# Kernel tuning notes

Measured on AMD Instinct MI355X. Metric: run time of the kernel, lower is better.

## Reference

```python
import jax, jax.numpy as jnp
import numpy as np

B, T, H = 8, 2048, 2048


def _wkv(key, value, time_decay, time_first):
    # key, value: [B, T, H]; time_decay/time_first: [H]
    u = time_first
    w = -jnp.exp(time_decay)  # negative decay per channel

    a0 = jnp.zeros(key.shape[::2], key.dtype)            # [B, H]
    b0 = jnp.zeros_like(a0)
    e0 = jnp.full_like(a0, -jnp.inf)

    def step(carry, kv):
        a, b, exponent = carry
        kt, vt = kv                                       # [B, H] each
        # output for this timestep (numerically stabilized)
        max_exp = jnp.maximum(exponent, u + kt)
        wt = jnp.exp(u + kt - max_exp)
        scale = jnp.exp(exponent - max_exp)
        wkv = (a * scale + wt * vt) / (b * scale + wt)
        # state update with decay w
        max_exp2 = jnp.maximum(exponent + w, kt)
        s1 = jnp.exp(exponent + w - max_exp2)
        s2 = jnp.exp(kt - max_exp2)
        a = s1 * a + s2 * vt
        b = s1 * b + s2
        return (a, b, max_exp2), wkv

    kT = jnp.swapaxes(key, 0, 1)    # [T, B, H] for scan over time
    vT = jnp.swapaxes(value, 0, 1)
    _, out = jax.lax.scan(step, (a0, b0, e0), (kT, vT))
    return jnp.swapaxes(out, 0, 1)  # [B, T, H]


def setup_inputs() -> dict:
    key = jax.random.key(0)
    k1, k2, k3, k4 = jax.random.split(key, 4)
    return {
        "key": jax.random.normal(k1, (B, T, H), jnp.float32),
        "value": jax.random.normal(k2, (B, T, H), jnp.float32),
        "time_decay": jax.random.normal(k3, (H,), jnp.float32) * 0.5,
        "time_first": jax.random.normal(k4, (H,), jnp.float32) * 0.5,
    }


def reference(key, value, time_decay, time_first):
    return _wkv(key, value, time_decay, time_first)
```

## Files before the change

kernel.cpp:

```cpp
#include <hip/hip_runtime.h>
#include <math.h>


#define WKV_B 8
#define WKV_T 2048
#define WKV_H 2048
#define WKV_BH (WKV_B * WKV_H)
#define WKV_U 8

__device__ __forceinline__ void wkv_update(float& a, float& bs, float& e,
                                           float w, float kt, float vt) {
    float ew = e + w;
    float m2 = fmaxf(ew, kt);
    float s1 = __expf(ew - m2);
    float s2 = __expf(kt - m2);
    a  = fmaf(s1, a, s2 * vt);
    bs = fmaf(s1, bs, s2);
    e  = m2;
}

__global__ __launch_bounds__(256)
void wkv_pass1(const float* __restrict__ k_, const float* __restrict__ v_,
               const float* __restrict__ td,
               float* __restrict__ pa, float* __restrict__ pb,
               float* __restrict__ pe, int L)
{
    const int ch = blockIdx.x * 256 + threadIdx.x;
    const int c  = blockIdx.y;
    const int h  = ch & (WKV_H - 1);
    const int b  = ch >> 11;
    const float w = -__expf(td[h]);

    const size_t base = (size_t)b * WKV_T * WKV_H + h + (size_t)c * L * WKV_H;
    const float* kp = k_ + base;
    const float* vp = v_ + base;

    float a = 0.0f, bs = 0.0f, e = -INFINITY;

    float kA[WKV_U], vA[WKV_U], kB[WKV_U], vB[WKV_U];
    #pragma unroll
    for (int i = 0; i < WKV_U; ++i) {
        kA[i] = kp[(size_t)i * WKV_H];
        vA[i] = vp[(size_t)i * WKV_H];
    }
    for (int t0 = 0; t0 < L; t0 += 2 * WKV_U) {
        #pragma unroll
        for (int i = 0; i < WKV_U; ++i) {
            kB[i] = kp[(size_t)(t0 + WKV_U + i) * WKV_H];
            vB[i] = vp[(size_t)(t0 + WKV_U + i) * WKV_H];
        }
        #pragma unroll
        for (int i = 0; i < WKV_U; ++i) wkv_update(a, bs, e, w, kA[i], vA[i]);
        if (t0 + 2 * WKV_U < L) {
            #pragma unroll
            for (int i = 0; i < WKV_U; ++i) {
                kA[i] = kp[(size_t)(t0 + 2 * WKV_U + i) * WKV_H];
                vA[i] = vp[(size_t)(t0 + 2 * WKV_U + i) * WKV_H];
            }
        }
        #pragma unroll
        for (int i = 0; i < WKV_U; ++i) wkv_update(a, bs, e, w, kB[i], vB[i]);
    }

    const size_t idx = (size_t)c * WKV_BH + ch;
    pa[idx] = a; pb[idx] = bs; pe[idx] = e;
}

__global__ __launch_bounds__(256)
void wkv_combine(float* __restrict__ pa, float* __restrict__ pb,
                 float* __restrict__ pe, const float* __restrict__ td,
                 int NC, int L)
{
    const int ch = blockIdx.x * 256 + threadIdx.x;
    const float w  = -__expf(td[ch & (WKV_H - 1)]);
    const float Lw = w * (float)L;

    float a = 0.0f, bs = 0.0f, e = -INFINITY;
    for (int c = 0; c < NC; ++c) {
        const size_t idx = (size_t)c * WKV_BH + ch;
        float qa = pa[idx], qb = pb[idx], qe = pe[idx];
        pa[idx] = a; pb[idx] = bs; pe[idx] = e;
        float ed = e + Lw;
        float m  = fmaxf(ed, qe);
        float s1 = __expf(ed - m);
        float s2 = __expf(qe - m);
        a  = fmaf(s1, a, s2 * qa);
        bs = fmaf(s1, bs, s2 * qb);
        e  = m;
    }
}

__global__ __launch_bounds__(256)
void wkv_pass3(const float* __restrict__ k_, const float* __restrict__ v_,
               const float* __restrict__ td, const float* __restrict__ tf,
               const float* __restrict__ pa, const float* __restrict__ pb,
               const float* __restrict__ pe,
               float* __restrict__ out, int L)
{
    const int ch = blockIdx.x * 256 + threadIdx.x;
    const int c  = blockIdx.y;
    const int h  = ch & (WKV_H - 1);
    const int b  = ch >> 11;
    const float u = tf[h];
    const float w = -__expf(td[h]);

    const size_t base = (size_t)b * WKV_T * WKV_H + h + (size_t)c * L * WKV_H;
    const float* kp = k_ + base;
    const float* vp = v_ + base;
    float*       op = out + base;

    const size_t idx = (size_t)c * WKV_BH + ch;
    float a = pa[idx], bs = pb[idx], e = pe[idx];

    auto step = [&](float kt, float vt, float* outp) {
        float uk  = u + kt;
        float m   = fmaxf(e, uk);
        float wt  = __expf(uk - m);
        float sc  = __expf(e - m);
        float num = fmaf(wt, vt, a * sc);
        float den = fmaf(bs, sc, wt);
        *outp = num * __builtin_amdgcn_rcpf(den);
        wkv_update(a, bs, e, w, kt, vt);
    };

    float kA[WKV_U], vA[WKV_U], kB[WKV_U], vB[WKV_U];
    #pragma unroll
    for (int i = 0; i < WKV_U; ++i) {
        kA[i] = kp[(size_t)i * WKV_H];
        vA[i] = vp[(size_t)i * WKV_H];
    }
    for (int t0 = 0; t0 < L; t0 += 2 * WKV_U) {
        #pragma unroll
        for (int i = 0; i < WKV_U; ++i) {
            kB[i] = kp[(size_t)(t0 + WKV_U + i) * WKV_H];
            vB[i] = vp[(size_t)(t0 + WKV_U + i) * WKV_H];
        }
        #pragma unroll
        for (int i = 0; i < WKV_U; ++i)
            step(kA[i], vA[i], op + (size_t)(t0 + i) * WKV_H);
        if (t0 + 2 * WKV_U < L) {
            #pragma unroll
            for (int i = 0; i < WKV_U; ++i) {
                kA[i] = kp[(size_t)(t0 + 2 * WKV_U + i) * WKV_H];
                vA[i] = vp[(size_t)(t0 + 2 * WKV_U + i) * WKV_H];
            }
        }
        #pragma unroll
        for (int i = 0; i < WKV_U; ++i)
            step(kB[i], vB[i], op + (size_t)(t0 + WKV_U + i) * WKV_H);
    }
}

extern "C" void kernel_launch(void* const* d_in, const int* in_sizes, int n_in,
                              void* d_out, int out_size, void* d_ws, size_t ws_size,
                              hipStream_t stream) {
    const float* key   = (const float*)d_in[0];
    const float* value = (const float*)d_in[1];
    const float* td    = (const float*)d_in[2];
    const float* tf    = (const float*)d_in[3];
    float* out = (float*)d_out;

    int NC = 32;
    while (NC > 1 && (size_t)3 * sizeof(float) * WKV_BH * NC > ws_size) NC >>= 1;
    const int L = WKV_T / NC;

    float* pa = (float*)d_ws;
    float* pb = pa + (size_t)WKV_BH * NC;
    float* pe = pb + (size_t)WKV_BH * NC;

    dim3 grid1(WKV_BH / 256, NC);
    wkv_pass1<<<grid1, 256, 0, stream>>>(key, value, td, pa, pb, pe, L);
    wkv_combine<<<WKV_BH / 256, 256, 0, stream>>>(pa, pb, pe, td, NC, L);
    wkv_pass3<<<grid1, 256, 0, stream>>>(key, value, td, tf, pa, pb, pe, out, L);
}
```

Before: 388.6 us.

## Stage key/value rows into LDS with async global_load_lds double buffering

Both scan passes now stage 8-timestep tiles of key and value into shared memory with direct global-to-LDS 16-byte loads, double-buffered and synchronised with explicit vmcnt waits and barriers. Each thread then reads its channel from LDS instead of issuing scalar per-timestep global loads. The aim is to keep more memory traffic in flight with wider loads and fewer registers, with an occupancy hint of 4 blocks per CU. The cost is block-wide barriers every sub-tile, and the hand-tuned vmcnt counts are fragile because pass3's output stores also count against vmcnt.

```diff
diff --git a/kernel.cpp b/kernel.cpp
--- a/kernel.cpp
+++ b/kernel.cpp
@@ -6,7 +6,11 @@
 #define WKV_T 2048
 #define WKV_H 2048
 #define WKV_BH (WKV_B * WKV_H)
-#define WKV_U 8
+#define G_CH 256
+#define SUB 8
+
+typedef const __attribute__((address_space(1))) void* gas_p;
+typedef __attribute__((address_space(3))) void* las_p;
 
 __device__ __forceinline__ void wkv_update(float& a, float& bs, float& e,
                                            float w, float kt, float vt) {
@@ -19,47 +23,62 @@
     e  = m2;
 }
 
-__global__ __launch_bounds__(256)
+__device__ __forceinline__ void stage_rows(const float* kbase, const float* vbase,
+                                           float (*kl)[G_CH], float (*vl)[G_CH],
+                                           int lane, int wid) {
+    #pragma unroll
+    for (int r = 0; r < 2; ++r) {
+        const int s = 2 * wid + r;
+        const float* gk = kbase + (size_t)s * WKV_H + lane * 4;
+        const float* gv = vbase + (size_t)s * WKV_H + lane * 4;
+        __builtin_amdgcn_global_load_lds((gas_p)gk, (las_p)&kl[s][0], 16, 0, 0);
+        __builtin_amdgcn_global_load_lds((gas_p)gv, (las_p)&vl[s][0], 16, 0, 0);
+    }
+}
+
+__global__ __launch_bounds__(256, 4)
 void wkv_pass1(const float* __restrict__ k_, const float* __restrict__ v_,
                const float* __restrict__ td,
                float* __restrict__ pa, float* __restrict__ pb,
                float* __restrict__ pe, int L)
 {
-    const int ch = blockIdx.x * 256 + threadIdx.x;
-    const int c  = blockIdx.y;
-    const int h  = ch & (WKV_H - 1);
-    const int b  = ch >> 11;
-    const float w = -__expf(td[h]);
+    __shared__ float kl[2][SUB][G_CH], vl[2][SUB][G_CH];
+    const int tid  = threadIdx.x, lane = tid & 63, wid = tid >> 6;
+    const int c    = blockIdx.y;
+    const int ch   = blockIdx.x * G_CH + tid;
+    const int h    = ch & (WKV_H - 1);
+    const int b    = ch >> 11;
 
-    const size_t base = (size_t)b * WKV_T * WKV_H + h + (size_t)c * L * WKV_H;
+    float w = -__expf(td[h]);
+    asm volatile("" : "+v"(w));
+
+    const size_t base = (size_t)b * WKV_T * WKV_H + (size_t)c * L * WKV_H
+                      + (size_t)(blockIdx.x * G_CH & (WKV_H - 1));
     const float* kp = k_ + base;
     const float* vp = v_ + base;
 
     float a = 0.0f, bs = 0.0f, e = -INFINITY;
+    const int NSUB = L / SUB;
 
-    float kA[WKV_U], vA[WKV_U], kB[WKV_U], vB[WKV_U];
-    #pragma unroll
-    for (int i = 0; i < WKV_U; ++i) {
-        kA[i] = kp[(size_t)i * WKV_H];
-        vA[i] = vp[(size_t)i * WKV_H];
-    }
-    for (int t0 = 0; t0 < L; t0 += 2 * WKV_U) {
+    stage_rows(kp, vp, kl[0], vl[0], lane, wid);
+    if (NSUB > 1)
+        stage_rows(kp + (size_t)SUB * WKV_H, vp + (size_t)SUB * WKV_H,
+                   kl[1], vl[1], lane, wid);
+
+    for (int s = 0; s < NSUB; ++s) {
+        if (s + 1 < NSUB) asm volatile("s_waitcnt vmcnt(4)" ::: "memory");
+        else              asm volatile("s_waitcnt vmcnt(0)" ::: "memory");
+        asm volatile("s_barrier" ::: "memory");
+        const int cur = s & 1;
         #pragma unroll
-        for (int i = 0; i < WKV_U; ++i) {
-            kB[i] = kp[(size_t)(t0 + WKV_U + i) * WKV_H];
-            vB[i] = vp[(size_t)(t0 + WKV_U + i) * WKV_H];
-        }
-        #pragma unroll
-        for (int i = 0; i < WKV_U; ++i) wkv_update(a, bs, e, w, kA[i], vA[i]);
-        if (t0 + 2 * WKV_U < L) {
-            #pragma unroll
-            for (int i = 0; i < WKV_U; ++i) {
-                kA[i] = kp[(size_t)(t0 + 2 * WKV_U + i) * WKV_H];
-                vA[i] = vp[(size_t)(t0 + 2 * WKV_U + i) * WKV_H];
-            }
-        }
-        #pragma unroll
-        for (int i = 0; i < WKV_U; ++i) wkv_update(a, bs, e, w, kB[i], vB[i]);
+        for (int i = 0; i < SUB; ++i)
+            wkv_update(a, bs, e, w, kl[cur][i][tid], vl[cur][i][tid]);
+        asm volatile("s_waitcnt lgkmcnt(0)" ::: "memory");
+        asm volatile("s_barrier" ::: "memory");
+        if (s + 2 < NSUB)
+            stage_rows(kp + (size_t)(s + 2) * SUB * WKV_H,
+                       vp + (size_t)(s + 2) * SUB * WKV_H,
+                       kl[cur], vl[cur], lane, wid);
     }
 
     const size_t idx = (size_t)c * WKV_BH + ch;
@@ -90,64 +109,64 @@
     }
 }
 
-__global__ __launch_bounds__(256)
+__global__ __launch_bounds__(256, 4)
 void wkv_pass3(const float* __restrict__ k_, const float* __restrict__ v_,
                const float* __restrict__ td, const float* __restrict__ tf,
                const float* __restrict__ pa, const float* __restrict__ pb,
                const float* __restrict__ pe,
                float* __restrict__ out, int L)
 {
-    const int ch = blockIdx.x * 256 + threadIdx.x;
-    const int c  = blockIdx.y;
-    const int h  = ch & (WKV_H - 1);
-    const int b  = ch >> 11;
-    const float u = tf[h];
-    const float w = -__expf(td[h]);
+    __shared__ float kl[2][SUB][G_CH], vl[2][SUB][G_CH];
+    const int tid  = threadIdx.x, lane = tid & 63, wid = tid >> 6;
+    const int c    = blockIdx.y;
+    const int ch   = blockIdx.x * G_CH + tid;
+    const int h    = ch & (WKV_H - 1);
+    const int b    = ch >> 11;
 
-    const size_t base = (size_t)b * WKV_T * WKV_H + h + (size_t)c * L * WKV_H;
+    const size_t idx = (size_t)c * WKV_BH + ch;
+    float u = tf[h];
+    float w = -__expf(td[h]);
+    float a = pa[idx], bs = pb[idx], e = pe[idx];
+    asm volatile("" : "+v"(u), "+v"(w), "+v"(a), "+v"(bs), "+v"(e));
+
+    const size_t base = (size_t)b * WKV_T * WKV_H + (size_t)c * L * WKV_H
+                      + (size_t)(blockIdx.x * G_CH & (WKV_H - 1));
     const float* kp = k_ + base;
     const float* vp = v_ + base;
-    float*       op = out + base;
+    float*       op = out + base + tid;
 
-    const size_t idx = (size_t)c * WKV_BH + ch;
-    float a = pa[idx], bs = pb[idx], e = pe[idx];
+    const int NSUB = L / SUB;
 
-    auto step = [&](float kt, float vt, float* outp) {
-        float uk  = u + kt;
-        float m   = fmaxf(e, uk);
-        float wt  = __expf(uk - m);
-        float sc  = __expf(e - m);
-        float num = fmaf(wt, vt, a * sc);
-        float den = fmaf(bs, sc, wt);
-        *outp = num * __builtin_amdgcn_rcpf(den);
-        wkv_update(a, bs, e, w, kt, vt);
-    };
+    stage_rows(kp, vp, kl[0], vl[0], lane, wid);
+    if (NSUB > 1)
+        stage_rows(kp + (size_t)SUB * WKV_H, vp + (size_t)SUB * WKV_H,
+                   kl[1], vl[1], lane, wid);
 
-    float kA[WKV_U], vA[WKV_U], kB[WKV_U], vB[WKV_U];
-    #pragma unroll
-    for (int i = 0; i < WKV_U; ++i) {
-        kA[i] = kp[(size_t)i * WKV_H];
-        vA[i] = vp[(size_t)i * WKV_H];
-    }
-    for (int t0 = 0; t0 < L; t0 += 2 * WKV_U) {
+    for (int s = 0; s < NSUB; ++s) {
+        if (s == 0)               asm volatile("s_waitcnt vmcnt(4)"  ::: "memory");
+        else if (s + 1 < NSUB)    asm volatile("s_waitcnt vmcnt(12)" ::: "memory");
+        else                      asm volatile("s_waitcnt vmcnt(0)"  ::: "memory");
+        asm volatile("s_barrier" ::: "memory");
+        const int cur = s & 1;
         #pragma unroll
-        for (int i = 0; i < WKV_U; ++i) {
-            kB[i] = kp[(size_t)(t0 + WKV_U + i) * WKV_H];
-            vB[i] = vp[(size_t)(t0 + WKV_U + i) * WKV_H];
+        for (int i = 0; i < SUB; ++i) {
+            float kt = kl[cur][i][tid];
+            float vt = vl[cur][i][tid];
+            float uk  = u + kt;
+            float m   = fmaxf(e, uk);
+            float wt  = __expf(uk - m);
+            float sc  = __expf(e - m);
+            float num = fmaf(wt, vt, a * sc);
+            float den = fmaf(bs, sc, wt);
+            op[(size_t)(s * SUB + i) * WKV_H] = num * __builtin_amdgcn_rcpf(den);
+            wkv_update(a, bs, e, w, kt, vt);
         }
-        #pragma unroll
-        for (int i = 0; i < WKV_U; ++i)
-            step(kA[i], vA[i], op + (size_t)(t0 + i) * WKV_H);
-        if (t0 + 2 * WKV_U < L) {
-            #pragma unroll
-            for (int i = 0; i < WKV_U; ++i) {
-                kA[i] = kp[(size_t)(t0 + 2 * WKV_U + i) * WKV_H];
-                vA[i] = vp[(size_t)(t0 + 2 * WKV_U + i) * WKV_H];
-            }
-        }
-        #pragma unroll
-        for (int i = 0; i < WKV_U; ++i)
-            step(kB[i], vB[i], op + (size_t)(t0 + WKV_U + i) * WKV_H);
+        asm volatile("s_waitcnt lgkmcnt(0)" ::: "memory");
+        asm volatile("s_barrier" ::: "memory");
+        if (s + 2 < NSUB)
+            stage_rows(kp + (size_t)(s + 2) * SUB * WKV_H,
+                       vp + (size_t)(s + 2) * SUB * WKV_H,
+                       kl[cur], vl[cur], lane, wid);
     }
 }
 
@@ -168,8 +187,8 @@
     float* pb = pa + (size_t)WKV_BH * NC;
     float* pe = pb + (size_t)WKV_BH * NC;
 
-    dim3 grid1(WKV_BH / 256, NC);
-    wkv_pass1<<<grid1, 256, 0, stream>>>(key, value, td, pa, pb, pe, L);
+    dim3 grid(WKV_BH / G_CH, NC);
+    wkv_pass1<<<grid, 256, 0, stream>>>(key, value, td, pa, pb, pe, L);
     wkv_combine<<<WKV_BH / 256, 256, 0, stream>>>(pa, pb, pe, td, NC, L);
-    wkv_pass3<<<grid1, 256, 0, stream>>>(key, value, td, tf, pa, pb, pe, out, L);
+    wkv_pass3<<<grid, 256, 0, stream>>>(key, value, td, tf, pa, pb, pe, out, L);
 }
```

Result: faster. 380.9 us (-2.0%).
